# Kernel tuning notes

Hardware: AMD Instinct MI355X
Metric: run time of the kernel (lower is better)

## Reference

```python
import jax, jax.numpy as jnp
import numpy as np
from math import factorial, sqrt

LMAX = 2
NB = 32
NRBF = 20
CUTOFF = 5.0
N_ATOMS = 20000
N_EDGES = 400000
T = 2
M = (LMAX + 1) ** 2
LIDX = np.repeat(np.arange(LMAX + 1), 2 * np.arange(LMAX + 1) + 1)  # l of each flat (l,m) index


def _cg_complex(j1, m1, j2, m2, j3, m3):
    # Racah formula for complex-SH Clebsch-Gordan coefficients
    if m3 != m1 + m2 or j3 < abs(j1 - j2) or j3 > j1 + j2:
        return 0.0
    f = factorial
    pref = sqrt((2 * j3 + 1) * f(j1 + j2 - j3) * f(j1 - j2 + j3) * f(-j1 + j2 + j3) / f(j1 + j2 + j3 + 1))
    pref *= sqrt(f(j1 + m1) * f(j1 - m1) * f(j2 + m2) * f(j2 - m2) * f(j3 + m3) * f(j3 - m3))
    kmin = max(0, j2 - j3 - m1, j1 + m2 - j3)
    kmax = min(j1 + j2 - j3, j1 - m1, j2 + m2)
    s = 0.0
    for k in range(kmin, kmax + 1):
        s += (-1) ** k / (f(k) * f(j1 + j2 - j3 - k) * f(j1 - m1 - k) * f(j2 + m2 - k) * f(j3 - j2 + m1 + k) * f(j3 - j1 - m2 + k))
    return pref * s


def _u_matrix(l):
    # real-SH = U @ complex-SH (rows: real m from -l..l, cols: complex m')
    U = np.zeros((2 * l + 1, 2 * l + 1), dtype=np.complex128)
    for m in range(-l, l + 1):
        if m == 0:
            U[l, l] = 1.0
        elif m > 0:
            U[l + m, l + m] = (-1) ** m / sqrt(2)
            U[l + m, l - m] = 1.0 / sqrt(2)
        else:
            mu = -m
            U[l + m, l + m] = 1j / sqrt(2)
            U[l + m, l - m] = -1j * (-1) ** mu / sqrt(2)
    return U


def _build_cg_rsh(lmax):
    # CG coefficients in the real-SH basis, parity invariant (odd l1+l2+l3 blocks zero)
    cg = np.zeros((M, M, M), dtype=np.float64)
    Us = [_u_matrix(l) for l in range(lmax + 1)]
    for l1 in range(lmax + 1):
        for l2 in range(lmax + 1):
            for l3 in range(lmax + 1):
                if (l1 + l2 + l3) % 2 == 1 or l3 < abs(l1 - l2) or l3 > l1 + l2:
                    continue
                Cc = np.zeros((2 * l1 + 1, 2 * l2 + 1, 2 * l3 + 1), dtype=np.complex128)
                for i, m1 in enumerate(range(-l1, l1 + 1)):
                    for j, m2 in enumerate(range(-l2, l2 + 1)):
                        m3 = m1 + m2
                        if abs(m3) <= l3:
                            Cc[i, j, l3 + m3] = _cg_complex(l1, m1, l2, m2, l3, m3)
                R = np.einsum('ai,bj,ck,ijk->abc', Us[l1], Us[l2], np.conj(Us[l3]), Cc)
                cg[l1 * l1:(l1 + 1) ** 2, l2 * l2:(l2 + 1) ** 2, l3 * l3:(l3 + 1) ** 2] = np.real(R)
    return cg.astype(np.float32)


CG = jnp.asarray(_build_cg_rsh(LMAX))   # [9, 9, 9]
LIDX_J = jnp.asarray(LIDX)


def _rsh(dirs):
    # real spherical harmonics up to l=2 on unit vectors, flat (l,m) order -> [P, 9]
    x, y, z = dirs[:, 0], dirs[:, 1], dirs[:, 2]
    c1 = 0.4886025119029199
    c2 = 1.0925484305920792
    return jnp.stack([
        jnp.full_like(x, 0.28209479177387814),
        c1 * y, c1 * z, c1 * x,
        c2 * x * y, c2 * y * z,
        0.31539156525252005 * (3.0 * z * z - 1.0),
        c2 * x * z,
        0.5462742152960396 * (x * x - y * y),
    ], axis=1)


def _forward(atomic_numbers, r_ij, idx_i, idx_j, emb, Wf, bf, Wm1, Wm2, Wm3, Wg, bg):
    d = jnp.linalg.norm(r_ij, axis=1)                      # [P]
    Y = _rsh(r_ij / d[:, None])                            # [P, 9]
    offsets = jnp.linspace(0.0, CUTOFF, NRBF)
    width = CUTOFF / (NRBF - 1)
    radial = jnp.exp(-0.5 / width ** 2 * (d[:, None] - offsets) ** 2)   # GaussianRBF [P, NRBF]
    fcut = jnp.where(d < CUTOFF, 0.5 * (jnp.cos(d * jnp.pi / CUTOFF) + 1.0), 0.0)  # CosineCutoff
    x0 = emb[atomic_numbers]                               # nuclear embedding [N, NB]
    x = jnp.concatenate([x0[:, None, :], jnp.zeros((x0.shape[0], M - 1, NB), x0.dtype)], axis=1)  # scalar2rsh
    for t in range(T):
        # SO3Convolution: per-edge radial filter per output degree l, cutoff gated
        Wl = ((radial @ Wf[t].T + bf[t]) * fcut[:, None]).reshape(-1, LMAX + 1, NB)
        xj = x[idx_j]                                      # gather neighbors [P, 9, NB]
        tbc = jnp.einsum('pa,abc->pbc', Y, CG)             # contract Y_ij with CG
        yij = jnp.einsum('pbc,pbn->pcn', tbc, xj) * Wl[:, LIDX_J, :]
        dx = jax.ops.segment_sum(yij, idx_i, num_segments=x.shape[0], indices_are_sorted=True)
        ddx = jnp.einsum('xcn,kn->xck', dx, Wm1[t])        # mixing1 (no bias)
        dx = dx + jnp.einsum('abc,xan,xbn->xcn', CG, dx, ddx)  # SO3TensorProduct
        dx = jnp.einsum('xcn,kn->xck', dx, Wm2[t])         # mixing2
        h = jax.nn.sigmoid((dx[:, 0, :] @ Wg[t].T + bg[t]).reshape(-1, LMAX + 1, NB))
        dx = dx * h[:, LIDX_J, :]                          # SO3ParametricGatedNonlinearity
        dx = jnp.einsum('xcn,kn->xck', dx, Wm3[t])         # mixing3
        x = x + dx
    return x                                               # multipole representation [N, 9, NB]


def setup_inputs():
    key = jax.random.key(0)
    ks = jax.random.split(key, 12)
    return {
        'atomic_numbers': jax.random.randint(ks[0], (N_ATOMS,), 1, 100),
        'r_ij': jax.random.normal(ks[1], (N_EDGES, 3), jnp.float32),
        'idx_i': jnp.sort(jax.random.randint(ks[2], (N_EDGES,), 0, N_ATOMS)),
        'idx_j': jax.random.randint(ks[3], (N_EDGES,), 0, N_ATOMS),
        'emb': jax.random.normal(ks[4], (101, NB), jnp.float32).at[0].set(0.0),
        'Wf': jax.random.normal(ks[5], (T, (LMAX + 1) * NB, NRBF), jnp.float32) / sqrt(NRBF),
        'bf': jnp.zeros((T, (LMAX + 1) * NB), jnp.float32),
        'Wm1': jax.random.normal(ks[6], (T, NB, NB), jnp.float32) / sqrt(NB),
        'Wm2': jax.random.normal(ks[7], (T, NB, NB), jnp.float32) / sqrt(NB),
        'Wm3': jax.random.normal(ks[8], (T, NB, NB), jnp.float32) / sqrt(NB),
        'Wg': jax.random.normal(ks[9], (T, (LMAX + 1) * NB, NB), jnp.float32) / sqrt(NB),
        'bg': jnp.zeros((T, (LMAX + 1) * NB), jnp.float32),
    }


def reference(atomic_numbers, r_ij, idx_i, idx_j, emb, Wf, bf, Wm1, Wm2, Wm3, Wg, bg):
    return _forward(atomic_numbers, r_ij, idx_i, idx_j, emb, Wf, bf, Wm1, Wm2, Wm3, Wg, bg)
```

## Files before the change

kernel.cpp:

```cpp
#include <hip/hip_runtime.h>

#define CHUNK 16

constexpr double CFACT[8] = {1.,1.,2.,6.,24.,120.,720.,5040.};

constexpr double csqrt(double x){
  if (x <= 0.0) return 0.0;
  double s = 1.0;
  while (x > 4.0)  { x *= 0.25; s *= 2.0; }
  while (x < 0.25) { x *= 4.0;  s *= 0.5; }
  double g = 1.0;
  for (int i=0;i<10;i++) g = 0.5*(g + x/g);
  return s*g;
}

constexpr double cg_complex(int j1,int m1,int j2,int m2,int j3,int m3){
  if (m3 != m1+m2 || j3 < (j1>j2?j1-j2:j2-j1) || j3 > j1+j2) return 0.0;
  double pref = csqrt((2.0*j3+1.0)*CFACT[j1+j2-j3]*CFACT[j1-j2+j3]*CFACT[-j1+j2+j3]/CFACT[j1+j2+j3+1]);
  pref *= csqrt(CFACT[j1+m1]*CFACT[j1-m1]*CFACT[j2+m2]*CFACT[j2-m2]*CFACT[j3+m3]*CFACT[j3-m3]);
  int kmin = 0;
  if (j2-j3-m1 > kmin) kmin = j2-j3-m1;
  if (j1+m2-j3 > kmin) kmin = j1+m2-j3;
  int kmax = j1+j2-j3;
  if (j1-m1 < kmax) kmax = j1-m1;
  if (j2+m2 < kmax) kmax = j2+m2;
  double s = 0.0;
  for (int k=kmin;k<=kmax;++k){
    double t = 1.0/(CFACT[k]*CFACT[j1+j2-j3-k]*CFACT[j1-m1-k]*CFACT[j2+m2-k]*CFACT[j3-j2+m1+k]*CFACT[j3-j1-m2+k]);
    s += (k&1)? -t : t;
  }
  return pref*s;
}

struct UR { int n; int mc[2]; double re[2]; double im[2]; };
constexpr UR u_row(int m){
  UR u{}; const double is2 = 0.70710678118654752440;
  if (m==0){ u.n=1; u.mc[0]=0; u.re[0]=1.0; u.im[0]=0.0; u.mc[1]=0; u.re[1]=0.0; u.im[1]=0.0; }
  else if (m>0){ u.n=2; u.mc[0]=m;  u.re[0]=((m&1)? -is2:is2); u.im[0]=0.0;
                        u.mc[1]=-m; u.re[1]=is2;               u.im[1]=0.0; }
  else { int mu=-m; u.n=2; u.mc[0]=m;  u.re[0]=0.0; u.im[0]=is2;
                           u.mc[1]=mu; u.re[1]=0.0; u.im[1]=((mu&1)? is2:-is2); }
  return u;
}

struct CGTab { float v[9][9][9]; };
constexpr CGTab build_cg(){
  CGTab g{};
  double cc[9][9][9] = {};
  for (int a=0;a<9;a++){
    int l1 = (a==0)?0:((a<4)?1:2); int m1 = a - (l1*l1+l1);
    for (int b=0;b<9;b++){
      int l2 = (b==0)?0:((b<4)?1:2); int m2 = b - (l2*l2+l2);
      int m3 = m1+m2;
      for (int l3=0;l3<=2;l3++){
        if (m3 < -l3 || m3 > l3) continue;
        cc[a][b][l3*l3+l3+m3] = cg_complex(l1,m1,l2,m2,l3,m3);
      }
    }
  }
  for (int l1=0;l1<=2;l1++) for (int l2=0;l2<=2;l2++) for (int l3=0;l3<=2;l3++){
    if (((l1+l2+l3)&1)==1) continue;
    int dl = (l1>l2)?(l1-l2):(l2-l1);
    if (l3 < dl || l3 > l1+l2) continue;
    for (int m1=-l1;m1<=l1;m1++) for (int m2=-l2;m2<=l2;m2++) for (int m3=-l3;m3<=l3;m3++){
      UR ua = u_row(m1), ub = u_row(m2), uc = u_row(m3);
      double acc = 0.0;
      for (int i=0;i<ua.n;i++) for (int j=0;j<ub.n;j++){
        double zr = ua.re[i]*ub.re[j] - ua.im[i]*ub.im[j];
        double zi = ua.re[i]*ub.im[j] + ua.im[i]*ub.re[j];
        for (int k=0;k<uc.n;k++){
          double rp = zr*uc.re[k] + zi*uc.im[k];
          if (rp != 0.0)
            acc += rp * cc[l1*l1+l1+ua.mc[i]][l2*l2+l2+ub.mc[j]][l3*l3+l3+uc.mc[k]];
        }
      }
      g.v[l1*l1+l1+m1][l2*l2+l2+m2][l3*l3+l3+m3] = (float)acc;
    }
  }
  return g;
}
constexpr CGTab CGT = build_cg();

__global__ void init_x_kernel(const int* __restrict__ Z, const float* __restrict__ emb,
                              float4* __restrict__ x4, float4* __restrict__ dx4, int n_atoms){
  int i = blockIdx.x*blockDim.x + threadIdx.x;
  if (i >= n_atoms*72) return;
  int atom = i/72, rem = i - atom*72;
  float4 v = make_float4(0.f,0.f,0.f,0.f);
  if (rem < 8) v = reinterpret_cast<const float4*>(emb)[Z[atom]*8 + rem];
  x4[i] = v;
  dx4[i] = make_float4(0.f,0.f,0.f,0.f);
}

template<bool FIRST>
__global__ __launch_bounds__(256, 1) void edge_kernel(
    const float* __restrict__ r_ij, const int* __restrict__ idx_i, const int* __restrict__ idx_j,
    const float* __restrict__ x, const float* __restrict__ Wf_t, const float* __restrict__ bf_t,
    float* __restrict__ dx, int n_edges)
{
  int tid = threadIdx.x;
  int g = tid >> 5, lane = tid & 31;
  int base = (blockIdx.x*8 + g)*CHUNK;
  if (base >= n_edges) return;
  const int nend = n_edges;

  float wfr[3][20]; float bfl[3];
  #pragma unroll
  for (int l=0;l<3;l++){
    const float* rp = Wf_t + (l*32+lane)*20;
    #pragma unroll
    for (int q=0;q<5;q++){
      float4 v4 = *reinterpret_cast<const float4*>(rp + q*4);
      wfr[l][q*4+0]=v4.x; wfr[l][q*4+1]=v4.y; wfr[l][q*4+2]=v4.z; wfr[l][q*4+3]=v4.w;
    }
    bfl[l] = bf_t[l*32+lane];
  }

  const float STEP  = 5.0f/19.0f;
  const float ALPHA = -0.5f/(STEP*STEP);
  float myoff = (float)lane * STEP;

  float racc[9];
  #pragma unroll
  for (int c=0;c<9;c++) racc[c]=0.f;
  int cur_i = -1;

  float xj[9]; float xj0;
  {
    int j0 = idx_j[base];
    const float* xp = x + j0*288 + lane;
    if (FIRST){ xj0 = xp[0]; }
    else {
      #pragma unroll
      for (int b=0;b<9;b++) xj[b] = xp[b*32];
    }
  }
  int e1 = (base+1 < nend) ? base+1 : nend-1;
  int j_next = idx_j[e1];

  #pragma unroll 2
  for (int k=0;k<CHUNK;k++){
    int e = base + k;
    if (e >= nend) break;

    float xjn[9]; float xjn0;
    {
      const float* xp = x + j_next*288 + lane;
      if (FIRST){ xjn0 = xp[0]; }
      else {
        #pragma unroll
        for (int b=0;b<9;b++) xjn[b] = xp[b*32];
      }
    }
    int en2 = (e+2 < nend) ? e+2 : nend-1;
    int j_n2 = idx_j[en2];

    int   ii = idx_i[e];
    float rx = r_ij[3*e+0], ry = r_ij[3*e+1], rz = r_ij[3*e+2];

    float d2 = fmaf(rx,rx,fmaf(ry,ry,rz*rz));
    float dd = sqrtf(d2);
    float inv = __fdividef(1.0f, dd);
    float X = rx*inv, Yv = ry*inv, Zv = rz*inv;
    const float c1 = 0.4886025119029199f, c2 = 1.0925484305920792f;
    float Y[9];
    Y[0]=0.28209479177387814f; Y[1]=c1*Yv; Y[2]=c1*Zv; Y[3]=c1*X;
    Y[4]=c2*X*Yv; Y[5]=c2*Yv*Zv; Y[6]=0.31539156525252005f*(3.f*Zv*Zv-1.f);
    Y[7]=c2*X*Zv; Y[8]=0.5462742152960396f*(X*X-Yv*Yv);

    float dtl = dd - myoff;
    float rbl = __expf(ALPHA*dtl*dtl);
    float wl0=bfl[0], wl1=bfl[1], wl2=bfl[2];
    #pragma unroll
    for (int r=0;r<20;r++){
      float rb = __shfl(rbl, r, 32);
      wl0 = fmaf(rb, wfr[0][r], wl0);
      wl1 = fmaf(rb, wfr[1][r], wl1);
      wl2 = fmaf(rb, wfr[2][r], wl2);
    }
    float fc = (dd < 5.0f) ? 0.5f*(__cosf(dd*0.6283185307179586f)+1.0f) : 0.0f;
    wl0*=fc; wl1*=fc; wl2*=fc;

    if (ii != cur_i){
      if (cur_i >= 0){
        float* dp = dx + cur_i*288 + lane;
        #pragma unroll
        for (int c=0;c<9;c++){ atomicAdd(dp + c*32, racc[c]); racc[c]=0.f; }
      }
      cur_i = ii;
    }

    if (FIRST){
      racc[0] = fmaf(wl0, Y[0]*xj0, racc[0]);
      #pragma unroll
      for (int c=1;c<4;c++) racc[c] = fmaf(wl1, Y[c]*xj0, racc[c]);
      #pragma unroll
      for (int c=4;c<9;c++) racc[c] = fmaf(wl2, Y[c]*xj0, racc[c]);
    } else {
      float yv[9];
      #pragma unroll
      for (int c=0;c<9;c++) yv[c]=0.f;
      #pragma unroll
      for (int a=0;a<9;a++){
        #pragma unroll
        for (int b=0;b<9;b++){
          bool any = false;
          #pragma unroll
          for (int c=0;c<9;c++) any = any | (CGT.v[a][b][c] != 0.f);
          if (any){
            float p = Y[a]*xj[b];
            #pragma unroll
            for (int c=0;c<9;c++){
              if (CGT.v[a][b][c] != 0.f) yv[c] = fmaf(CGT.v[a][b][c], p, yv[c]);
            }
          }
        }
      }
      racc[0] = fmaf(wl0, yv[0], racc[0]);
      #pragma unroll
      for (int c=1;c<4;c++) racc[c] = fmaf(wl1, yv[c], racc[c]);
      #pragma unroll
      for (int c=4;c<9;c++) racc[c] = fmaf(wl2, yv[c], racc[c]);
    }

    j_next = j_n2;
    if (FIRST){ xj0 = xjn0; }
    else {
      #pragma unroll
      for (int b=0;b<9;b++) xj[b] = xjn[b];
    }
  }
  if (cur_i >= 0){
    float* dp = dx + cur_i*288 + lane;
    #pragma unroll
    for (int c=0;c<9;c++) atomicAdd(dp + c*32, racc[c]);
  }
}

__global__ __launch_bounds__(256) void atom_kernel(
    float* __restrict__ x, float* __restrict__ dxg,
    const float* __restrict__ Wm1_t, const float* __restrict__ Wm2_t, const float* __restrict__ Wm3_t,
    const float* __restrict__ Wg_t, const float* __restrict__ bg_t, int n_atoms)
{
  __shared__ __align__(16) float tile[8][288];
  int tid = threadIdx.x;
  int g = tid>>5, k = tid&31;
  int atom = blockIdx.x*8 + g;
  if (atom >= n_atoms) return;
  float* tg = &tile[g][0];
  const float4* t4 = reinterpret_cast<const float4*>(tg);

  float* dp = dxg + atom*288 + k;
  float v[9];
  #pragma unroll
  for (int c=0;c<9;c++){ v[c]=dp[c*32]; tg[c*32+k]=v[c]; dp[c*32]=0.f; }

  float wr[32];
  {
    const float4* w4 = reinterpret_cast<const float4*>(Wm1_t + k*32);
    #pragma unroll
    for (int q=0;q<8;q++){ float4 a=w4[q]; wr[4*q]=a.x; wr[4*q+1]=a.y; wr[4*q+2]=a.z; wr[4*q+3]=a.w; }
  }
  float u[9];
  #pragma unroll
  for (int c=0;c<9;c++){
    float s=0.f;
    #pragma unroll
    for (int q=0;q<8;q++){
      float4 tv = t4[c*8+q];
      s = fmaf(tv.x, wr[4*q+0], s); s = fmaf(tv.y, wr[4*q+1], s);
      s = fmaf(tv.z, wr[4*q+2], s); s = fmaf(tv.w, wr[4*q+3], s);
    }
    u[c]=s;
  }

  float w[9];
  #pragma unroll
  for (int c=0;c<9;c++) w[c]=v[c];
  #pragma unroll
  for (int a=0;a<9;a++){
    #pragma unroll
    for (int b=0;b<9;b++){
      bool any = false;
      #pragma unroll
      for (int c=0;c<9;c++) any = any | (CGT.v[a][b][c] != 0.f);
      if (any){
        float p = v[a]*u[b];
        #pragma unroll
        for (int c=0;c<9;c++){
          if (CGT.v[a][b][c] != 0.f) w[c] = fmaf(CGT.v[a][b][c], p, w[c]);
        }
      }
    }
  }

  #pragma unroll
  for (int c=0;c<9;c++) tg[c*32+k]=w[c];
  {
    const float4* w4 = reinterpret_cast<const float4*>(Wm2_t + k*32);
    #pragma unroll
    for (int q=0;q<8;q++){ float4 a=w4[q]; wr[4*q]=a.x; wr[4*q+1]=a.y; wr[4*q+2]=a.z; wr[4*q+3]=a.w; }
  }
  float p[9];
  #pragma unroll
  for (int c=0;c<9;c++){
    float s=0.f;
    #pragma unroll
    for (int q=0;q<8;q++){
      float4 tv = t4[c*8+q];
      s = fmaf(tv.x, wr[4*q+0], s); s = fmaf(tv.y, wr[4*q+1], s);
      s = fmaf(tv.z, wr[4*q+2], s); s = fmaf(tv.w, wr[4*q+3], s);
    }
    p[c]=s;
  }

  tg[k] = p[0];
  float s0=bg_t[k], s1=bg_t[32+k], s2=bg_t[64+k];
  {
    const float4* wg0 = reinterpret_cast<const float4*>(Wg_t + (     k)*32);
    const float4* wg1 = reinterpret_cast<const float4*>(Wg_t + (32 + k)*32);
    const float4* wg2 = reinterpret_cast<const float4*>(Wg_t + (64 + k)*32);
    #pragma unroll
    for (int q=0;q<8;q++){
      float4 tv = t4[q];
      float4 a0 = wg0[q], a1 = wg1[q], a2 = wg2[q];
      s0 = fmaf(tv.x,a0.x,s0); s0 = fmaf(tv.y,a0.y,s0); s0 = fmaf(tv.z,a0.z,s0); s0 = fmaf(tv.w,a0.w,s0);
      s1 = fmaf(tv.x,a1.x,s1); s1 = fmaf(tv.y,a1.y,s1); s1 = fmaf(tv.z,a1.z,s1); s1 = fmaf(tv.w,a1.w,s1);
      s2 = fmaf(tv.x,a2.x,s2); s2 = fmaf(tv.y,a2.y,s2); s2 = fmaf(tv.z,a2.z,s2); s2 = fmaf(tv.w,a2.w,s2);
    }
  }
  float h0 = 1.f/(1.f+__expf(-s0));
  float h1 = 1.f/(1.f+__expf(-s1));
  float h2 = 1.f/(1.f+__expf(-s2));

  float q9[9];
  q9[0]=p[0]*h0;
  #pragma unroll
  for (int c=1;c<4;c++) q9[c]=p[c]*h1;
  #pragma unroll
  for (int c=4;c<9;c++) q9[c]=p[c]*h2;

  #pragma unroll
  for (int c=0;c<9;c++) tg[c*32+k]=q9[c];
  {
    const float4* w4 = reinterpret_cast<const float4*>(Wm3_t + k*32);
    #pragma unroll
    for (int q=0;q<8;q++){ float4 a=w4[q]; wr[4*q]=a.x; wr[4*q+1]=a.y; wr[4*q+2]=a.z; wr[4*q+3]=a.w; }
  }
  float* xo = x + atom*288 + k;
  #pragma unroll
  for (int c=0;c<9;c++){
    float s=0.f;
    #pragma unroll
    for (int q=0;q<8;q++){
      float4 tv = t4[c*8+q];
      s = fmaf(tv.x, wr[4*q+0], s); s = fmaf(tv.y, wr[4*q+1], s);
      s = fmaf(tv.z, wr[4*q+2], s); s = fmaf(tv.w, wr[4*q+3], s);
    }
    xo[c*32] += s;
  }
}

extern "C" void kernel_launch(void* const* d_in, const int* in_sizes, int n_in,
                              void* d_out, int out_size, void* d_ws, size_t ws_size,
                              hipStream_t stream)
{
  const int*   Z    = (const int*)d_in[0];
  const float* r_ij = (const float*)d_in[1];
  const int*   idxi = (const int*)d_in[2];
  const int*   idxj = (const int*)d_in[3];
  const float* emb  = (const float*)d_in[4];
  const float* Wf   = (const float*)d_in[5];
  const float* bf   = (const float*)d_in[6];
  const float* Wm1  = (const float*)d_in[7];
  const float* Wm2  = (const float*)d_in[8];
  const float* Wm3  = (const float*)d_in[9];
  const float* Wg   = (const float*)d_in[10];
  const float* bg   = (const float*)d_in[11];
  int n_atoms = in_sizes[0];
  int n_edges = in_sizes[1]/3;

  float* x  = (float*)d_out;
  float* dx = (float*)d_ws;

  init_x_kernel<<<(n_atoms*72+255)/256,256,0,stream>>>(Z, emb, (float4*)x, (float4*)dx, n_atoms);

  int eblocks = (n_edges + 8*CHUNK - 1)/(8*CHUNK);
  int ablocks = (n_atoms + 7)/8;

  edge_kernel<true><<<eblocks,256,0,stream>>>(r_ij, idxi, idxj, x, Wf, bf, dx, n_edges);
  atom_kernel<<<ablocks,256,0,stream>>>(x, dx, Wm1, Wm2, Wm3, Wg, bg, n_atoms);

  edge_kernel<false><<<eblocks,256,0,stream>>>(r_ij, idxi, idxj, x,
                                        Wf + 96*20, bf + 96, dx, n_edges);
  atom_kernel<<<ablocks,256,0,stream>>>(x, dx,
                                        Wm1 + 1024, Wm2 + 1024, Wm3 + 1024,
                                        Wg + 96*32, bg + 96, n_atoms);
}
```

Before: 405.9 us.

## Split edge pass into precomputed geometry/radial-weight tables and a lean scatter kernel

Spherical harmonics per edge and cutoff-scaled radial filter weights per interaction are computed in separate dense kernels and written to workspace tables. A lean edge kernel then reads these tables, gathers neighbour features and scatters into atoms, with a smaller chunk size and no single-block occupancy bound. The aim is to take the radial MLP and transcendental work off the latency-bound gather/atomic kernel so it can run at higher occupancy. In exchange it adds extra launches and writes and reads about 400 bytes per edge of table traffic per interaction. The new path runs only when the workspace is large enough.

```diff
diff --git a/kernel.cpp b/kernel.cpp
--- a/kernel.cpp
+++ b/kernel.cpp
@@ -1,6 +1,7 @@
 #include <hip/hip_runtime.h>
 
-#define CHUNK 16
+#define CHUNK  16
+#define ECHUNK 8
 
 constexpr double CFACT[8] = {1.,1.,2.,6.,24.,120.,720.,5040.};
 
@@ -92,8 +93,178 @@
   dx4[i] = make_float4(0.f,0.f,0.f,0.f);
 }
 
+__global__ __launch_bounds__(256) void geom_kernel(const float* __restrict__ r_ij,
+                                                   float* __restrict__ Yt, int n_edges){
+  int e = blockIdx.x*256 + threadIdx.x;
+  if (e >= n_edges) return;
+  float rx = r_ij[3*e+0], ry = r_ij[3*e+1], rz = r_ij[3*e+2];
+  float d2 = fmaf(rx,rx,fmaf(ry,ry,rz*rz));
+  float inv = __frsqrt_rn(d2);
+  float X = rx*inv, Yv = ry*inv, Zv = rz*inv;
+  const float c1 = 0.4886025119029199f, c2 = 1.0925484305920792f;
+  float4* o = reinterpret_cast<float4*>(Yt + e*12);
+  o[0] = make_float4(0.28209479177387814f, c1*Yv, c1*Zv, c1*X);
+  o[1] = make_float4(c2*X*Yv, c2*Yv*Zv, 0.31539156525252005f*(3.f*Zv*Zv-1.f), c2*X*Zv);
+  o[2] = make_float4(0.5462742152960396f*(X*X-Yv*Yv), 0.f, 0.f, 0.f);
+}
+
+__global__ __launch_bounds__(256) void wl_kernel(const float* __restrict__ r_ij,
+                                                 const float* __restrict__ Wf_t,
+                                                 const float* __restrict__ bf_t,
+                                                 float* __restrict__ Wlt, int n_edges){
+  int tid = threadIdx.x;
+  int g = tid >> 5, lane = tid & 31;
+  int e = blockIdx.x*8 + g;
+  if (e >= n_edges) return;
+
+  float wfr[3][20]; float bfl[3];
+  #pragma unroll
+  for (int l=0;l<3;l++){
+    const float* rp = Wf_t + (l*32+lane)*20;
+    #pragma unroll
+    for (int q=0;q<5;q++){
+      float4 v4 = *reinterpret_cast<const float4*>(rp + q*4);
+      wfr[l][q*4+0]=v4.x; wfr[l][q*4+1]=v4.y; wfr[l][q*4+2]=v4.z; wfr[l][q*4+3]=v4.w;
+    }
+    bfl[l] = bf_t[l*32+lane];
+  }
+
+  float rx = r_ij[3*e+0], ry = r_ij[3*e+1], rz = r_ij[3*e+2];
+  float dd = sqrtf(fmaf(rx,rx,fmaf(ry,ry,rz*rz)));
+
+  const float STEP  = 5.0f/19.0f;
+  const float ALPHA = -0.5f/(STEP*STEP);
+  float dtl = dd - (float)lane*STEP;
+  float rbl = __expf(ALPHA*dtl*dtl);
+
+  float wl0=bfl[0], wl1=bfl[1], wl2=bfl[2];
+  #pragma unroll
+  for (int r=0;r<20;r++){
+    float rb = __shfl(rbl, r, 32);
+    wl0 = fmaf(rb, wfr[0][r], wl0);
+    wl1 = fmaf(rb, wfr[1][r], wl1);
+    wl2 = fmaf(rb, wfr[2][r], wl2);
+  }
+  float fc = (dd < 5.0f) ? 0.5f*(__cosf(dd*0.6283185307179586f)+1.0f) : 0.0f;
+  float* op = Wlt + e*96 + lane;
+  op[0]  = wl0*fc;
+  op[32] = wl1*fc;
+  op[64] = wl2*fc;
+}
+
 template<bool FIRST>
-__global__ __launch_bounds__(256, 1) void edge_kernel(
+__global__ __launch_bounds__(256) void edge_lean_kernel(
+    const float* __restrict__ Yt, const float* __restrict__ Wlt,
+    const int* __restrict__ idx_i, const int* __restrict__ idx_j,
+    const float* __restrict__ x, float* __restrict__ dx, int n_edges)
+{
+  int tid = threadIdx.x;
+  int g = tid >> 5, lane = tid & 31;
+  int base = (blockIdx.x*8 + g)*ECHUNK;
+  if (base >= n_edges) return;
+  const int nend = n_edges;
+
+  float racc[9];
+  #pragma unroll
+  for (int c=0;c<9;c++) racc[c]=0.f;
+  int cur_i = -1;
+
+  float xj[9]; float xj0 = 0.f;
+  {
+    int j0 = idx_j[base];
+    const float* xp = x + j0*288 + lane;
+    if (FIRST){ xj0 = xp[0]; }
+    else {
+      #pragma unroll
+      for (int b=0;b<9;b++) xj[b] = xp[b*32];
+    }
+  }
+  int e1 = (base+1 <= nend-1) ? base+1 : nend-1;
+  int j_next = idx_j[e1];
+
+  #pragma unroll 2
+  for (int k=0;k<ECHUNK;k++){
+    int e = base + k;
+    if (e >= nend) break;
+
+    float xjn[9]; float xjn0 = 0.f;
+    {
+      const float* xp = x + j_next*288 + lane;
+      if (FIRST){ xjn0 = xp[0]; }
+      else {
+        #pragma unroll
+        for (int b=0;b<9;b++) xjn[b] = xp[b*32];
+      }
+    }
+    int en2 = (e+2 <= nend-1) ? e+2 : nend-1;
+    int j_n2 = idx_j[en2];
+
+    int ii = idx_i[e];
+    const float* wp = Wlt + e*96 + lane;
+    float wl0 = wp[0], wl1 = wp[32], wl2 = wp[64];
+    const float* yp = Yt + e*12;
+    float Y[9];
+    #pragma unroll
+    for (int c=0;c<9;c++) Y[c] = yp[c];
+
+    if (ii != cur_i){
+      if (cur_i >= 0){
+        float* dp = dx + cur_i*288 + lane;
+        #pragma unroll
+        for (int c=0;c<9;c++){ atomicAdd(dp + c*32, racc[c]); racc[c]=0.f; }
+      }
+      cur_i = ii;
+    }
+
+    if (FIRST){
+      racc[0] = fmaf(wl0, Y[0]*xj0, racc[0]);
+      #pragma unroll
+      for (int c=1;c<4;c++) racc[c] = fmaf(wl1, Y[c]*xj0, racc[c]);
+      #pragma unroll
+      for (int c=4;c<9;c++) racc[c] = fmaf(wl2, Y[c]*xj0, racc[c]);
+    } else {
+      float yv[9];
+      #pragma unroll
+      for (int c=0;c<9;c++) yv[c]=0.f;
+      #pragma unroll
+      for (int a=0;a<9;a++){
+        #pragma unroll
+        for (int b=0;b<9;b++){
+          bool any = false;
+          #pragma unroll
+          for (int c=0;c<9;c++) any = any | (CGT.v[a][b][c] != 0.f);
+          if (any){
+            float p = Y[a]*xj[b];
+            #pragma unroll
+            for (int c=0;c<9;c++){
+              if (CGT.v[a][b][c] != 0.f) yv[c] = fmaf(CGT.v[a][b][c], p, yv[c]);
+            }
+          }
+        }
+      }
+      racc[0] = fmaf(wl0, yv[0], racc[0]);
+      #pragma unroll
+      for (int c=1;c<4;c++) racc[c] = fmaf(wl1, yv[c], racc[c]);
+      #pragma unroll
+      for (int c=4;c<9;c++) racc[c] = fmaf(wl2, yv[c], racc[c]);
+    }
+
+    j_next = j_n2;
+    if (FIRST){ xj0 = xjn0; }
+    else {
+      #pragma unroll
+      for (int b=0;b<9;b++) xj[b] = xjn[b];
+    }
+  }
+  if (cur_i >= 0){
+    float* dp = dx + cur_i*288 + lane;
+    #pragma unroll
+    for (int c=0;c<9;c++) atomicAdd(dp + c*32, racc[c]);
+  }
+}
+
+template<bool FIRST>
+__global__ __launch_bounds__(256) void edge_kernel(
     const float* __restrict__ r_ij, const int* __restrict__ idx_i, const int* __restrict__ idx_j,
     const float* __restrict__ x, const float* __restrict__ Wf_t, const float* __restrict__ bf_t,
     float* __restrict__ dx, int n_edges)
@@ -125,7 +296,7 @@
   for (int c=0;c<9;c++) racc[c]=0.f;
   int cur_i = -1;
 
-  float xj[9]; float xj0;
+  float xj[9]; float xj0 = 0.f;
   {
     int j0 = idx_j[base];
     const float* xp = x + j0*288 + lane;
@@ -135,7 +306,7 @@
       for (int b=0;b<9;b++) xj[b] = xp[b*32];
     }
   }
-  int e1 = (base+1 < nend) ? base+1 : nend-1;
+  int e1 = (base+1 <= nend-1) ? base+1 : nend-1;
   int j_next = idx_j[e1];
 
   #pragma unroll 2
@@ -143,7 +314,7 @@
     int e = base + k;
     if (e >= nend) break;
 
-    float xjn[9]; float xjn0;
+    float xjn[9]; float xjn0 = 0.f;
     {
       const float* xp = x + j_next*288 + lane;
       if (FIRST){ xjn0 = xp[0]; }
@@ -152,7 +323,7 @@
         for (int b=0;b<9;b++) xjn[b] = xp[b*32];
       }
     }
-    int en2 = (e+2 < nend) ? e+2 : nend-1;
+    int en2 = (e+2 <= nend-1) ? e+2 : nend-1;
     int j_n2 = idx_j[en2];
 
     int   ii = idx_i[e];
@@ -383,17 +554,40 @@
   float* x  = (float*)d_out;
   float* dx = (float*)d_ws;
 
+  size_t dxB = (size_t)n_atoms*288*sizeof(float);
+  size_t YB  = (size_t)n_edges*12*sizeof(float);
+  size_t WlB = (size_t)n_edges*96*sizeof(float);
+  bool tables = (ws_size >= dxB + YB + WlB);
+
   init_x_kernel<<<(n_atoms*72+255)/256,256,0,stream>>>(Z, emb, (float4*)x, (float4*)dx, n_atoms);
 
-  int eblocks = (n_edges + 8*CHUNK - 1)/(8*CHUNK);
   int ablocks = (n_atoms + 7)/8;
 
-  edge_kernel<true><<<eblocks,256,0,stream>>>(r_ij, idxi, idxj, x, Wf, bf, dx, n_edges);
-  atom_kernel<<<ablocks,256,0,stream>>>(x, dx, Wm1, Wm2, Wm3, Wg, bg, n_atoms);
-
-  edge_kernel<false><<<eblocks,256,0,stream>>>(r_ij, idxi, idxj, x,
-                                        Wf + 96*20, bf + 96, dx, n_edges);
-  atom_kernel<<<ablocks,256,0,stream>>>(x, dx,
-                                        Wm1 + 1024, Wm2 + 1024, Wm3 + 1024,
-                                        Wg + 96*32, bg + 96, n_atoms);
-}
+  if (tables){
+    float* Yt  = (float*)((char*)d_ws + dxB);
+    float* Wlt = (float*)((char*)d_ws + dxB + YB);
+    int gblocks = (n_edges + 255)/256;
+    int wblocks = (n_edges + 7)/8;
+    int lblocks = (n_edges + 8*ECHUNK - 1)/(8*ECHUNK);
+
+    geom_kernel<<<gblocks,256,0,stream>>>(r_ij, Yt, n_edges);
+
+    wl_kernel<<<wblocks,256,0,stream>>>(r_ij, Wf, bf, Wlt, n_edges);
+    edge_lean_kernel<true><<<lblocks,256,0,stream>>>(Yt, Wlt, idxi, idxj, x, dx, n_edges);
+    atom_kernel<<<ablocks,256,0,stream>>>(x, dx, Wm1, Wm2, Wm3, Wg, bg, n_atoms);
+
+    wl_kernel<<<wblocks,256,0,stream>>>(r_ij, Wf + 96*20, bf + 96, Wlt, n_edges);
+    edge_lean_kernel<false><<<lblocks,256,0,stream>>>(Yt, Wlt, idxi, idxj, x, dx, n_edges);
+    atom_kernel<<<ablocks,256,0,stream>>>(x, dx, Wm1 + 1024, Wm2 + 1024, Wm3 + 1024,
+                                          Wg + 96*32, bg + 96, n_atoms);
+  } else {
+    int eblocks = (n_edges + 8*CHUNK - 1)/(8*CHUNK);
+    edge_kernel<true><<<eblocks,256,0,stream>>>(r_ij, idxi, idxj, x, Wf, bf, dx, n_edges);
+    atom_kernel<<<ablocks,256,0,stream>>>(x, dx, Wm1, Wm2, Wm3, Wg, bg, n_atoms);
+    edge_kernel<false><<<eblocks,256,0,stream>>>(r_ij, idxi, idxj, x,
+                                          Wf + 96*20, bf + 96, dx, n_edges);
+    atom_kernel<<<ablocks,256,0,stream>>>(x, dx,
+                                          Wm1 + 1024, Wm2 + 1024, Wm3 + 1024,
+                                          Wg + 96*32, bg + 96, n_atoms);
+  }
+}
```

Result: slower. 686.6 us (+69.2%).
